# Optimization experiments

Hardware: AMD Instinct MI355X
Metric: run time of the kernel (lower is better)

## Reference

```python
import jax, jax.numpy as jnp
import numpy as np

B, Q, K, H, DV = 16, 256, 256, 256, 256


def setup_inputs() -> dict:
    key = jax.random.key(0)
    ks = jax.random.split(key, 6)
    return {
        "queries": jax.random.normal(ks[0], (B, Q, H), dtype=jnp.float32),
        "keys": jax.random.normal(ks[1], (B, K, H), dtype=jnp.float32),
        "values": jax.random.normal(ks[2], (B, K, DV), dtype=jnp.float32),
        "W_q": jax.random.normal(ks[3], (H, H), dtype=jnp.float32) / np.sqrt(H),
        "W_k": jax.random.normal(ks[4], (H, H), dtype=jnp.float32) / np.sqrt(H),
        "w_v": jax.random.normal(ks[5], (H,), dtype=jnp.float32) / np.sqrt(H),
    }


def reference(queries, keys, values, W_q, W_k, w_v):
    # Linear projections (nn.Linear: x @ W.T), bias-free
    q = jnp.einsum("bqd,hd->bqh", queries, W_q)  # [B,Q,H]
    k = jnp.einsum("bkd,hd->bkh", keys, W_k)      # [B,K,H]
    # Broadcast add -> tanh -> scalar projection
    features = jnp.tanh(q[:, :, None, :] + k[:, None, :, :])  # [B,Q,K,H]
    scores = jnp.einsum("bqkh,h->bqk", features, w_v)          # [B,Q,K]
    attn = jax.nn.softmax(scores, axis=-1)                      # [B,Q,K]
    return jnp.einsum("bqk,bkv->bqv", attn, values)            # [B,Q,DV]
```

## Files before the change

### kernel.cpp

```cpp
#include <hip/hip_runtime.h>

#define Bn 16
#define Qn 256
#define Kn 256
#define Hn 256
#define DVn 256

constexpr float C2    = 2.8853900817779268f;
constexpr float LOG2E = 1.4426950408889634f;

typedef __attribute__((ext_vector_type(8))) short bf16x8;
typedef __attribute__((ext_vector_type(4))) float f32x4;

__device__ __forceinline__ float fast_exp2(float x) { return __builtin_amdgcn_exp2f(x); }
__device__ __forceinline__ float fast_rcp(float x)  { return __builtin_amdgcn_rcpf(x); }

__device__ __forceinline__ unsigned short f2bf(float x) {
    unsigned u = __float_as_uint(x);
    u += 0x7fffu + ((u >> 16) & 1u);
    return (unsigned short)(u >> 16);
}

__device__ __forceinline__ bf16x8 cvt8(const float* p) {
    float4 x0 = *(const float4*)p;
    float4 x1 = *(const float4*)(p + 4);
    bf16x8 r;
    r[0] = (short)f2bf(x0.x); r[1] = (short)f2bf(x0.y);
    r[2] = (short)f2bf(x0.z); r[3] = (short)f2bf(x0.w);
    r[4] = (short)f2bf(x1.x); r[5] = (short)f2bf(x1.y);
    r[6] = (short)f2bf(x1.z); r[7] = (short)f2bf(x1.w);
    return r;
}

__global__ __launch_bounds__(256)
void proj_mfma_kernel(const float* __restrict__ q, const float* __restrict__ kx,
                      const float* __restrict__ wq, const float* __restrict__ wk,
                      const float* __restrict__ V,
                      float* __restrict__ Eq, unsigned short* __restrict__ Ekb,
                      float* __restrict__ Vp)
{
    const int tid  = threadIdx.x;
    const int wvid = tid >> 6, lane = tid & 63;
    const int bid  = blockIdx.x;
    const int m0   = (bid >> 1) * 16;
    const int n0   = (bid & 1) * 128 + wvid * 32;
    const bool isQ = (m0 < 4096);
    const int r16  = lane & 15, q8 = (lane >> 4) * 8;

    const float* Xrow = (isQ ? q + (size_t)(m0 + r16) * 256
                             : kx + (size_t)(m0 - 4096 + r16) * 256) + q8;
    bf16x8 afr[8];
    #pragma unroll
    for (int s = 0; s < 8; ++s) afr[s] = cvt8(Xrow + s * 32);

    const float* Wbase = isQ ? wq : wk;
    f32x4 acc[2];
    #pragma unroll
    for (int nt = 0; nt < 2; ++nt) {
        const float* Wrow = Wbase + (size_t)(n0 + nt * 16 + r16) * 256 + q8;
        f32x4 c = {0.f, 0.f, 0.f, 0.f};
        #pragma unroll
        for (int s = 0; s < 8; ++s) {
            bf16x8 bfr = cvt8(Wrow + s * 32);
            c = __builtin_amdgcn_mfma_f32_16x16x32_bf16(afr[s], bfr, c, 0, 0, 0);
        }
        acc[nt] = c;
    }
    const int rbase = (lane >> 4) * 4;
    #pragma unroll
    for (int nt = 0; nt < 2; ++nt) {
        const int n = n0 + nt * 16 + r16;
        #pragma unroll
        for (int r = 0; r < 4; ++r) {
            const int m = m0 + rbase + r;
            const float val = fast_exp2(C2 * acc[nt][r]);
            if (isQ) {
                Eq[(size_t)m * 256 + n] = val;
            } else {
                const int kr = m - 4096, b = kr >> 8, kk = kr & 255;
                Ekb[(((size_t)(b * 64 + (n >> 2))) * 256 + kk) * 4 + (n & 3)] = f2bf(val);
            }
        }
    }
    {
        const int p   = bid * 256 + tid;
        const int bk4 = p >> 8, dv = p & 255;
        const int b   = bk4 >> 6, k4 = bk4 & 63;
        const float* src = V + ((size_t)(b * Kn + 4 * k4)) * DVn + dv;
        float4 o;
        o.x = src[0 * DVn]; o.y = src[1 * DVn]; o.z = src[2 * DVn]; o.w = src[3 * DVn];
        *(float4*)(Vp + (size_t)p * 4) = o;
    }
}

__global__ __launch_bounds__(256, 4)
void fused_attn_kernel(const float* __restrict__ Eq, const unsigned short* __restrict__ Ekb,
                       const float* __restrict__ wv, const float* __restrict__ Vp,
                       float* __restrict__ out)
{
    const int b   = blockIdx.y;
    const int q0  = blockIdx.x * 4;
    const int tid = threadIdx.x;

    __shared__ __align__(16) float sEq[4 * 256];
    __shared__ __align__(16) float sWv[256];
    __shared__ __align__(16) float sPv[256 * 4];
    __shared__ float sredM[4][4];
    __shared__ float sredS[4][4];

    {
        const float* eqb = Eq + (size_t)(b * Qn + q0) * Hn;
        const int qq = tid >> 6, h4 = (tid & 63) * 4;
        *(float4*)&sEq[qq * 256 + h4] = *(const float4*)(eqb + qq * 256 + h4);
        if (tid < 64) *(float4*)&sWv[tid * 4] = *(const float4*)(wv + tid * 4);
    }
    __syncthreads();

    float sc[4] = {0.f, 0.f, 0.f, 0.f};
    const uint2* ekp = (const uint2*)Ekb + (size_t)b * 16384 + tid;
    uint2 e[4];
    #pragma unroll
    for (int g = 0; g < 4; ++g) e[g] = ekp[g * 256];
    for (int it = 0; it < 16; ++it) {
        uint2 en[4];
        if (it < 15) {
            #pragma unroll
            for (int g = 0; g < 4; ++g) en[g] = ekp[(4 * (it + 1) + g) * 256];
        }
        const int h0 = it * 16;
        #pragma unroll
        for (int g = 0; g < 4; ++g) {
            float ek0 = __uint_as_float(e[g].x << 16);
            float ek1 = __uint_as_float(e[g].x & 0xFFFF0000u);
            float ek2 = __uint_as_float(e[g].y << 16);
            float ek3 = __uint_as_float(e[g].y & 0xFFFF0000u);
            const float4 wa = *(const float4*)&sWv[h0 + 4 * g];
            #pragma unroll
            for (int qq = 0; qq < 4; ++qq) {
                const float4 ea = *(const float4*)&sEq[qq * 256 + h0 + 4 * g];
                float a = sc[qq];
                a = fmaf(wa.x, fast_rcp(fmaf(ea.x, ek0, 1.f)), a);
                a = fmaf(wa.y, fast_rcp(fmaf(ea.y, ek1, 1.f)), a);
                a = fmaf(wa.z, fast_rcp(fmaf(ea.z, ek2, 1.f)), a);
                a = fmaf(wa.w, fast_rcp(fmaf(ea.w, ek3, 1.f)), a);
                sc[qq] = a;
            }
        }
        #pragma unroll
        for (int g = 0; g < 4; ++g) e[g] = en[g];
    }

    const int w = tid >> 6, lane = tid & 63;
    #pragma unroll
    for (int qq = 0; qq < 4; ++qq) {
        sc[qq] = -2.0f * sc[qq];
        float mx = sc[qq];
        #pragma unroll
        for (int off = 32; off; off >>= 1) mx = fmaxf(mx, __shfl_xor(mx, off, 64));
        if (lane == 0) sredM[qq][w] = mx;
    }
    __syncthreads();
    float pq[4];
    #pragma unroll
    for (int qq = 0; qq < 4; ++qq) {
        const float mx = fmaxf(fmaxf(sredM[qq][0], sredM[qq][1]),
                               fmaxf(sredM[qq][2], sredM[qq][3]));
        pq[qq] = fast_exp2(LOG2E * (sc[qq] - mx));
        float s = pq[qq];
        #pragma unroll
        for (int off = 32; off; off >>= 1) s += __shfl_xor(s, off, 64);
        if (lane == 0) sredS[qq][w] = s;
    }
    *(float4*)&sPv[tid * 4] = make_float4(pq[0], pq[1], pq[2], pq[3]);
    __syncthreads();
    float rinv[4];
    #pragma unroll
    for (int qq = 0; qq < 4; ++qq)
        rinv[qq] = fast_rcp(sredS[qq][0] + sredS[qq][1] + sredS[qq][2] + sredS[qq][3]);

    float acc[4] = {0.f, 0.f, 0.f, 0.f};
    const float4* vp = (const float4*)Vp + (size_t)b * 64 * 256 + tid;
    float4 vv = vp[0];
    for (int k4 = 0; k4 < 64; ++k4) {
        float4 vn;
        if (k4 < 63) vn = vp[(k4 + 1) * 256];
        const float vj[4] = {vv.x, vv.y, vv.z, vv.w};
        #pragma unroll
        for (int j = 0; j < 4; ++j) {
            const float4 p4 = *(const float4*)&sPv[(4 * k4 + j) * 4];
            acc[0] = fmaf(p4.x, vj[j], acc[0]);
            acc[1] = fmaf(p4.y, vj[j], acc[1]);
            acc[2] = fmaf(p4.z, vj[j], acc[2]);
            acc[3] = fmaf(p4.w, vj[j], acc[3]);
        }
        vv = vn;
    }
    float* ob = out + (size_t)(b * Qn + q0) * DVn + tid;
    ob[0 * DVn] = acc[0] * rinv[0];
    ob[1 * DVn] = acc[1] * rinv[1];
    ob[2 * DVn] = acc[2] * rinv[2];
    ob[3 * DVn] = acc[3] * rinv[3];
}

extern "C" void kernel_launch(void* const* d_in, const int* in_sizes, int n_in,
                              void* d_out, int out_size, void* d_ws, size_t ws_size,
                              hipStream_t stream) {
    const float* queries = (const float*)d_in[0];
    const float* keys    = (const float*)d_in[1];
    const float* values  = (const float*)d_in[2];
    const float* W_q     = (const float*)d_in[3];
    const float* W_k     = (const float*)d_in[4];
    const float* w_v     = (const float*)d_in[5];
    float* out = (float*)d_out;

    float*          Eq  = (float*)d_ws;
    unsigned short* Ekb = (unsigned short*)(Eq + (size_t)Bn * Qn * Hn);
    float*          Vp  = (float*)(Ekb + (size_t)Bn * Kn * Hn);

    proj_mfma_kernel<<<dim3(1024), 256, 0, stream>>>(queries, keys, W_q, W_k, values,
                                                     Eq, Ekb, Vp);
    fused_attn_kernel<<<dim3(64, 16), 256, 0, stream>>>(Eq, Ekb, w_v, Vp, out);
}
```

Before: 136.7 us.

## Pair reciprocals in tanh-score loop with packed FMA and fp32 key exponentials

Rewrites the inner score loop so two reciprocal terms w0/A0 + w1/A1 are combined into one reciprocal of A0*A1 with a cross-multiplied numerator, halving transcendental rcp instructions, and uses two-wide packed FMAs for the denominators. The key exponentials are stored as fp32 instead of bf16, which doubles that buffer's traffic but removes the unpack shifts. The -2 scale is folded into w_v. It also splits accumulation into two independent chains. The risk is overflow or precision loss when the product of two large exp terms exceeds fp32 range.

```diff
diff --git a/kernel.cpp b/kernel.cpp
--- a/kernel.cpp
+++ b/kernel.cpp
@@ -11,9 +11,18 @@
 
 typedef __attribute__((ext_vector_type(8))) short bf16x8;
 typedef __attribute__((ext_vector_type(4))) float f32x4;
+typedef __attribute__((ext_vector_type(2))) float f32x2;
 
 __device__ __forceinline__ float fast_exp2(float x) { return __builtin_amdgcn_exp2f(x); }
 __device__ __forceinline__ float fast_rcp(float x)  { return __builtin_amdgcn_rcpf(x); }
+
+__device__ __forceinline__ f32x2 fma2(f32x2 a, f32x2 b, f32x2 c) {
+#if __has_builtin(__builtin_elementwise_fma)
+    return __builtin_elementwise_fma(a, b, c);
+#else
+    f32x2 r; r.x = fmaf(a.x, b.x, c.x); r.y = fmaf(a.y, b.y, c.y); return r;
+#endif
+}
 
 __device__ __forceinline__ unsigned short f2bf(float x) {
     unsigned u = __float_as_uint(x);
@@ -36,7 +45,7 @@
 void proj_mfma_kernel(const float* __restrict__ q, const float* __restrict__ kx,
                       const float* __restrict__ wq, const float* __restrict__ wk,
                       const float* __restrict__ V,
-                      float* __restrict__ Eq, unsigned short* __restrict__ Ekb,
+                      float* __restrict__ Eq, float* __restrict__ Ekf,
                       float* __restrict__ Vp)
 {
     const int tid  = threadIdx.x;
@@ -78,7 +87,7 @@
                 Eq[(size_t)m * 256 + n] = val;
             } else {
                 const int kr = m - 4096, b = kr >> 8, kk = kr & 255;
-                Ekb[(((size_t)(b * 64 + (n >> 2))) * 256 + kk) * 4 + (n & 3)] = f2bf(val);
+                Ekf[(((size_t)(b * 64 + (n >> 2))) * 256 + kk) * 4 + (n & 3)] = val;
             }
         }
     }
@@ -94,7 +103,7 @@
 }
 
 __global__ __launch_bounds__(256, 4)
-void fused_attn_kernel(const float* __restrict__ Eq, const unsigned short* __restrict__ Ekb,
+void fused_attn_kernel(const float* __restrict__ Eq, const float* __restrict__ Ekf,
                        const float* __restrict__ wv, const float* __restrict__ Vp,
                        float* __restrict__ out)
 {
@@ -112,17 +121,22 @@
         const float* eqb = Eq + (size_t)(b * Qn + q0) * Hn;
         const int qq = tid >> 6, h4 = (tid & 63) * 4;
         *(float4*)&sEq[qq * 256 + h4] = *(const float4*)(eqb + qq * 256 + h4);
-        if (tid < 64) *(float4*)&sWv[tid * 4] = *(const float4*)(wv + tid * 4);
+        if (tid < 64) {
+            float4 wvec = *(const float4*)(wv + tid * 4);
+            wvec.x *= -2.f; wvec.y *= -2.f; wvec.z *= -2.f; wvec.w *= -2.f;
+            *(float4*)&sWv[tid * 4] = wvec;
+        }
     }
     __syncthreads();
 
-    float sc[4] = {0.f, 0.f, 0.f, 0.f};
-    const uint2* ekp = (const uint2*)Ekb + (size_t)b * 16384 + tid;
-    uint2 e[4];
+    float acc0[4] = {0.f, 0.f, 0.f, 0.f};
+    float acc1[4] = {0.f, 0.f, 0.f, 0.f};
+    const float4* ekp = (const float4*)Ekf + (size_t)b * 16384 + tid;
+    float4 e[4];
     #pragma unroll
     for (int g = 0; g < 4; ++g) e[g] = ekp[g * 256];
     for (int it = 0; it < 16; ++it) {
-        uint2 en[4];
+        float4 en[4];
         if (it < 15) {
             #pragma unroll
             for (int g = 0; g < 4; ++g) en[g] = ekp[(4 * (it + 1) + g) * 256];
@@ -130,30 +144,32 @@
         const int h0 = it * 16;
         #pragma unroll
         for (int g = 0; g < 4; ++g) {
-            float ek0 = __uint_as_float(e[g].x << 16);
-            float ek1 = __uint_as_float(e[g].x & 0xFFFF0000u);
-            float ek2 = __uint_as_float(e[g].y << 16);
-            float ek3 = __uint_as_float(e[g].y & 0xFFFF0000u);
-            const float4 wa = *(const float4*)&sWv[h0 + 4 * g];
+            const float4 ekq = e[g];
+            const float4 wa  = *(const float4*)&sWv[h0 + 4 * g];
+            const f32x2 ek01 = {ekq.x, ekq.y};
+            const f32x2 ek23 = {ekq.z, ekq.w};
+            const f32x2 one2 = {1.f, 1.f};
             #pragma unroll
             for (int qq = 0; qq < 4; ++qq) {
                 const float4 ea = *(const float4*)&sEq[qq * 256 + h0 + 4 * g];
-                float a = sc[qq];
-                a = fmaf(wa.x, fast_rcp(fmaf(ea.x, ek0, 1.f)), a);
-                a = fmaf(wa.y, fast_rcp(fmaf(ea.y, ek1, 1.f)), a);
-                a = fmaf(wa.z, fast_rcp(fmaf(ea.z, ek2, 1.f)), a);
-                a = fmaf(wa.w, fast_rcp(fmaf(ea.w, ek3, 1.f)), a);
-                sc[qq] = a;
+                const f32x2 A01 = fma2((f32x2){ea.x, ea.y}, ek01, one2);
+                const f32x2 A23 = fma2((f32x2){ea.z, ea.w}, ek23, one2);
+                const float num0 = fmaf(wa.x, A01.y, wa.y * A01.x);
+                const float num1 = fmaf(wa.z, A23.y, wa.w * A23.x);
+                acc0[qq] = fmaf(num0, fast_rcp(A01.x * A01.y), acc0[qq]);
+                acc1[qq] = fmaf(num1, fast_rcp(A23.x * A23.y), acc1[qq]);
             }
         }
         #pragma unroll
         for (int g = 0; g < 4; ++g) e[g] = en[g];
     }
 
+    float sc[4];
+    #pragma unroll
+    for (int qq = 0; qq < 4; ++qq) sc[qq] = acc0[qq] + acc1[qq];
     const int w = tid >> 6, lane = tid & 63;
     #pragma unroll
     for (int qq = 0; qq < 4; ++qq) {
-        sc[qq] = -2.0f * sc[qq];
         float mx = sc[qq];
         #pragma unroll
         for (int off = 32; off; off >>= 1) mx = fmaxf(mx, __shfl_xor(mx, off, 64));
@@ -213,11 +229,11 @@
     const float* w_v     = (const float*)d_in[5];
     float* out = (float*)d_out;
 
-    float*          Eq  = (float*)d_ws;
-    unsigned short* Ekb = (unsigned short*)(Eq + (size_t)Bn * Qn * Hn);
-    float*          Vp  = (float*)(Ekb + (size_t)Bn * Kn * Hn);
+    float* Eq  = (float*)d_ws;
+    float* Ekf = Eq + (size_t)Bn * Qn * Hn;
+    float* Vp  = Ekf + (size_t)Bn * Kn * Hn;
 
     proj_mfma_kernel<<<dim3(1024), 256, 0, stream>>>(queries, keys, W_q, W_k, values,
-                                                     Eq, Ekb, Vp);
-    fused_attn_kernel<<<dim3(64, 16), 256, 0, stream>>>(Eq, Ekb, w_v, Vp, out);
-}
+                                                     Eq, Ekf, Vp);
+    fused_attn_kernel<<<dim3(64, 16), 256, 0, stream>>>(Eq, Ekf, w_v, Vp, out);
+}
```

Result: slower. 157.8 us (+15.4%).
